# Performance work log

Measured on AMD Instinct MI355X. Metric: run time of the kernel, lower is better.

Reference implementation:

```python
import jax, jax.numpy as jnp
import numpy as np

N_USERS = 100000
N_ITEMS = 50000
N = N_USERS + N_ITEMS
EMB_DIM = 64
N_LAYERS = 3
NNZ = 6400000
BATCH = 4096


def setup_inputs() -> dict:
    key = jax.random.key(0)
    k = jax.random.split(key, 7)
    user_emb = 0.1 * jax.random.normal(k[0], (N_USERS, EMB_DIM), dtype=jnp.float32)
    item_emb = 0.1 * jax.random.normal(k[1], (N_ITEMS, EMB_DIM), dtype=jnp.float32)
    graph_val = jax.random.uniform(k[2], (NNZ,), dtype=jnp.float32) * 0.05
    graph_src = jax.random.randint(k[3], (NNZ,), 0, N, dtype=jnp.int64) if jax.config.jax_enable_x64 else jax.random.randint(k[3], (NNZ,), 0, N).astype(jnp.int32)
    graph_dst = jax.random.randint(k[4], (NNZ,), 0, N).astype(graph_src.dtype)
    users = jax.random.randint(k[5], (BATCH,), 0, N_USERS).astype(graph_src.dtype)
    items = jax.random.randint(k[6], (BATCH,), 0, N_ITEMS).astype(graph_src.dtype)
    return {"user_emb": user_emb, "item_emb": item_emb, "graph_val": graph_val,
            "graph_src": graph_src, "graph_dst": graph_dst, "users": users, "items": items}


def _spmm(val, src, dst, x):
    # y[src] += val * x[dst]  -- sparse (COO) matrix @ dense
    return jax.ops.segment_sum(val[:, None] * x[dst], src, num_segments=N)


def reference(user_emb, item_emb, graph_val, graph_src, graph_dst, users, items):
    all_emb = jnp.concatenate([user_emb, item_emb], axis=0)  # [N, d]
    acc = all_emb  # running sum over layers (fused mean accumulation)
    x = all_emb
    for _ in range(N_LAYERS):
        x = _spmm(graph_val, graph_src, graph_dst, x)
        acc = acc + x
    light_out = acc / (N_LAYERS + 1)
    all_users = light_out[:N_USERS]
    all_items = light_out[N_USERS:]
    scores = jnp.sum(all_users[users] * all_items[items], axis=1)  # [B]
    return scores
```

## Files before the change

kernel.cpp:

```cpp
#include <hip/hip_runtime.h>


constexpr int N_USERS = 100000;
constexpr int N_ITEMS = 50000;
constexpr int N_NODES = N_USERS + N_ITEMS;
constexpr int EMB = 64;
constexpr int NNZ = 6400000;
constexpr int BATCH = 4096;

constexpr int BSHIFT = 9;
constexpr int BWIDTH = 1 << BSHIFT;
constexpr int NB = (N_NODES + BWIDTH - 1) >> BSHIFT;
constexpr int NBPAD = 512;
constexpr int BSTRIDE = 23500;
constexpr int PBSTRIDE = 26624;

constexpr int TILE = 5120;
constexpr int P1_BLOCKS = NNZ / TILE;
constexpr int EPT1 = TILE / 256;

constexpr float QSCALE = 327680.0f;
constexpr float QINV   = 1.0f / 327680.0f;

struct h4 { _Float16 x, y, z, w; };
typedef _Float16 half8v __attribute__((ext_vector_type(8)));

__global__ void gcur_init_kernel(int* __restrict__ gcur) {
    int i = blockIdx.x * blockDim.x + threadIdx.x;
    if (i < NB) gcur[i] = i * BSTRIDE;
}

__global__ void p1_bin_kernel(const int* __restrict__ src, const int* __restrict__ dst,
                              const float* __restrict__ val, int* __restrict__ gcur,
                              uint2* __restrict__ staging) {
    __shared__ int hist[NBPAD];
    __shared__ int gbase[NBPAD];
    __shared__ int cur[NBPAD];
    __shared__ int sbuf[NBPAD];
    __shared__ int lbase[NBPAD];
    __shared__ uint2 ebuf[TILE];
    int t = threadIdx.x;
    int tile = blockIdx.x * TILE;
    int srcs[EPT1];
    #pragma unroll
    for (int k = 0; k < EPT1; ++k) srcs[k] = src[tile + t + k * 256];
    for (int i = t; i < NBPAD; i += 256) { hist[i] = 0; cur[i] = 0; }
    __syncthreads();
    #pragma unroll
    for (int k = 0; k < EPT1; ++k) atomicAdd(&hist[srcs[k] >> BSHIFT], 1);
    __syncthreads();
    for (int i = t; i < NB; i += 256) {
        int h = hist[i];
        gbase[i] = (h > 0) ? atomicAdd(&gcur[i], h) : 0;
    }
    for (int i = t; i < NBPAD; i += 256) sbuf[i] = hist[i];
    __syncthreads();
    int* pin = sbuf; int* pout = lbase;
    for (int off = 1; off < NBPAD; off <<= 1) {
        for (int i = t; i < NBPAD; i += 256) {
            int v = pin[i];
            if (i >= off) v += pin[i - off];
            pout[i] = v;
        }
        __syncthreads();
        int* tmp = pin; pin = pout; pout = tmp;
    }
    for (int i = t; i < NBPAD; i += 256) lbase[i] = pin[i] - hist[i];
    __syncthreads();
    #pragma unroll
    for (int k = 0; k < EPT1; ++k) {
        int i = tile + t + k * 256;
        int s = srcs[k];
        int b = s >> BSHIFT;
        int c = atomicAdd(&cur[b], 1);
        int d = dst[i];
        float v = val[i];
        unsigned q = (unsigned)(v * QSCALE);
        if (q > 16383u) q = 16383u;
        ebuf[lbase[b] + c] = make_uint2((q << 18) | (unsigned)d, (unsigned)s);
    }
    __syncthreads();
    #pragma unroll
    for (int k = 0; k < EPT1; ++k) {
        int j = t + k * 256;
        uint2 e = ebuf[j];
        int b = (int)(e.y >> BSHIFT);
        unsigned pos = (unsigned)(gbase[b] + (j - lbase[b]));
        if (pos < (unsigned)((b + 1) * BSTRIDE))
            staging[pos] = e;
    }
}

__global__ void p2_sort_kernel(const int* __restrict__ gcur, const uint2* __restrict__ staging,
                               unsigned* __restrict__ epack, unsigned* __restrict__ prow) {
    __shared__ int hist[BWIDTH], sA[BWIDTH], sB[BWIDTH], cur[BWIDTH];
    int b = blockIdx.x;
    int t = threadIdx.x;
    int cnt = gcur[b] - b * BSTRIDE;
    if (cnt > BSTRIDE) cnt = BSTRIDE;
    int sbase = b * BSTRIDE;
    for (int i = t; i < BWIDTH; i += 256) hist[i] = 0;
    __syncthreads();
    for (int j = t; j < cnt; j += 256) {
        uint2 e = staging[sbase + j];
        atomicAdd(&hist[e.y & (BWIDTH - 1)], 1);
    }
    __syncthreads();
    for (int i = t; i < BWIDTH; i += 256) sA[i] = (hist[i] + 7) >> 3;
    __syncthreads();
    int* pin = sA; int* pout = sB;
    for (int off = 1; off < BWIDTH; off <<= 1) {
        for (int i = t; i < BWIDTH; i += 256) {
            int v = pin[i];
            if (i >= off) v += pin[i - off];
            pout[i] = v;
        }
        __syncthreads();
        int* tmp = pin; pin = pout; pout = tmp;
    }
    for (int i = t; i < BWIDTH; i += 256) {
        int pw = (hist[i] + 7) >> 3;
        int ps = pin[i] - pw;
        unsigned poff = (unsigned)(b * PBSTRIDE + 8 * ps);
        int fit = (PBSTRIDE - 8 * ps) >> 3;
        if (fit < 0) fit = 0;
        if (pw > fit) pw = fit;
        if (pw > 15) pw = 15;
        cur[i] = (int)poff;
        int node = (b << BSHIFT) + i;
        if (node < N_NODES) prow[node] = (poff << 4) | (unsigned)pw;
    }
    __syncthreads();
    unsigned bend = (unsigned)((b + 1) * PBSTRIDE);
    for (int j = t; j < cnt; j += 256) {
        uint2 e = staging[sbase + j];
        int p = atomicAdd(&cur[e.y & (BWIDTH - 1)], 1);
        if ((unsigned)p < bend) epack[p] = e.x;
    }
}

__global__ void init_kernel(const float4* __restrict__ ue, const float4* __restrict__ ie,
                            h4* __restrict__ x) {
    int i = blockIdx.x * blockDim.x + threadIdx.x;
    const int total = N_NODES * (EMB / 4);
    if (i >= total) return;
    const int usplit = N_USERS * (EMB / 4);
    float4 v = (i < usplit) ? ue[i] : ie[i - usplit];
    x[i] = h4{(_Float16)v.x, (_Float16)v.y, (_Float16)v.z, (_Float16)v.w};
}

__global__ void gather_init_kernel(const float* __restrict__ ue, const float* __restrict__ ie,
                                   const int* __restrict__ users, const int* __restrict__ items,
                                   float* __restrict__ accb) {
    int gid = blockIdx.x * blockDim.x + threadIdx.x;
    int w = gid >> 6;
    int lane = threadIdx.x & 63;
    if (w >= BATCH * 2) return;
    int b = w >> 1;
    float v;
    if (w & 1) v = ie[(long long)items[b] * EMB + lane];
    else       v = ue[(long long)users[b] * EMB + lane];
    accb[(long long)w * EMB + lane] = v;
}

__global__ void gather_add_kernel(const _Float16* __restrict__ x, const int* __restrict__ users,
                                  const int* __restrict__ items, float* __restrict__ accb) {
    int gid = blockIdx.x * blockDim.x + threadIdx.x;
    int w = gid >> 6;
    int lane = threadIdx.x & 63;
    if (w >= BATCH * 2) return;
    int b = w >> 1;
    int node = (w & 1) ? (N_USERS + items[b]) : users[b];
    accb[(long long)w * EMB + lane] += (float)x[(unsigned)node * EMB + lane];
}

__device__ __forceinline__ void row_gather_p8(unsigned pr, int lane,
                                              const unsigned* __restrict__ epack,
                                              const _Float16* __restrict__ x,
                                              float acc[8]) {
    const int l8 = lane & 7;
    const int qb = lane & 56;
    const unsigned li8b = (unsigned)l8 * 16u;
    float a0 = 0, a1 = 0, a2 = 0, a3 = 0, a4 = 0, a5 = 0, a6 = 0, a7 = 0;
    float b0 = 0, b1 = 0, b2 = 0, b3 = 0, b4 = 0, b5 = 0, b6 = 0, b7 = 0;
    const unsigned* ep = epack + (pr >> 4);
    const char* xb = (const char*)x;
    int nwin = (int)(pr & 15u);
    if (nwin > 0) {
        unsigned e = ep[l8];
        for (int w = 0; w < nwin; ++w) {
            unsigned en = ep[8 + l8];
            ep += 8;
            unsigned voff = (e & 0x3FFFFu) << 7;
            float v = ((float)(e >> 18) + 0.5f) * QINV;
            #pragma unroll
            for (int t = 0; t < 8; t += 2) {
                unsigned offA = (unsigned)__shfl((int)voff, qb + t, 64);
                unsigned offB = (unsigned)__shfl((int)voff, qb + t + 1, 64);
                float vA = __shfl(v, qb + t, 64);
                float vB = __shfl(v, qb + t + 1, 64);
                const half8v hA = *(const half8v*)(xb + (offA | li8b));
                const half8v hB = *(const half8v*)(xb + (offB | li8b));
                a0 += vA * (float)hA[0];  a1 += vA * (float)hA[1];
                a2 += vA * (float)hA[2];  a3 += vA * (float)hA[3];
                a4 += vA * (float)hA[4];  a5 += vA * (float)hA[5];
                a6 += vA * (float)hA[6];  a7 += vA * (float)hA[7];
                b0 += vB * (float)hB[0];  b1 += vB * (float)hB[1];
                b2 += vB * (float)hB[2];  b3 += vB * (float)hB[3];
                b4 += vB * (float)hB[4];  b5 += vB * (float)hB[5];
                b6 += vB * (float)hB[6];  b7 += vB * (float)hB[7];
            }
            e = en;
        }
    }
    acc[0] = a0 + b0; acc[1] = a1 + b1; acc[2] = a2 + b2; acc[3] = a3 + b3;
    acc[4] = a4 + b4; acc[5] = a5 + b5; acc[6] = a6 + b6; acc[7] = a7 + b7;
}

__global__ void spmm_full_kernel(const unsigned* __restrict__ prow,
                                 const unsigned* __restrict__ epack,
                                 const _Float16* __restrict__ x, _Float16* __restrict__ y) {
    int gid = blockIdx.x * blockDim.x + threadIdx.x;
    int row = gid >> 3;
    if (row >= N_NODES) return;
    int lane = threadIdx.x & 63;
    float acc[8];
    row_gather_p8(prow[row], lane, epack, x, acc);
    half8v h;
    #pragma unroll
    for (int i = 0; i < 8; ++i) h[i] = (_Float16)acc[i];
    *(half8v*)(y + ((unsigned)row << 6) + (unsigned)(lane & 7) * 8) = h;
}

__global__ void spmm_sel_kernel(const unsigned* __restrict__ prow,
                                const unsigned* __restrict__ epack,
                                const _Float16* __restrict__ x, const int* __restrict__ users,
                                const int* __restrict__ items, float* __restrict__ accb) {
    int gid = blockIdx.x * blockDim.x + threadIdx.x;
    int g = gid >> 3;
    if (g >= BATCH * 2) return;
    int lane = threadIdx.x & 63;
    int b = g >> 1;
    int node = (g & 1) ? (N_USERS + items[b]) : users[b];
    float acc[8];
    row_gather_p8(prow[node], lane, epack, x, acc);
    float4* p = (float4*)(accb + ((long long)g << 6) + (lane & 7) * 8);
    float4 c0 = p[0], c1 = p[1];
    c0.x += acc[0]; c0.y += acc[1]; c0.z += acc[2]; c0.w += acc[3];
    c1.x += acc[4]; c1.y += acc[5]; c1.z += acc[6]; c1.w += acc[7];
    p[0] = c0; p[1] = c1;
}

__global__ void score_kernel(const float* __restrict__ accb, float* __restrict__ out) {
    int gid = blockIdx.x * blockDim.x + threadIdx.x;
    int b = gid >> 6;
    int lane = threadIdx.x & 63;
    if (b >= BATCH) return;
    float a = accb[(long long)(2 * b) * EMB + lane];
    float c = accb[(long long)(2 * b + 1) * EMB + lane];
    float p = a * c;
    #pragma unroll
    for (int off = 32; off > 0; off >>= 1) p += __shfl_down(p, off, 64);
    if (lane == 0) out[b] = p * (1.0f / 16.0f);
}

extern "C" void kernel_launch(void* const* d_in, const int* in_sizes, int n_in,
                              void* d_out, int out_size, void* d_ws, size_t ws_size,
                              hipStream_t stream) {
    const float* user_emb  = (const float*)d_in[0];
    const float* item_emb  = (const float*)d_in[1];
    const float* graph_val = (const float*)d_in[2];
    const int*   graph_src = (const int*)d_in[3];
    const int*   graph_dst = (const int*)d_in[4];
    const int*   users     = (const int*)d_in[5];
    const int*   items     = (const int*)d_in[6];
    float* out = (float*)d_out;

    char* base = (char*)d_ws;
    const size_t STAGE_BYTES = (size_t)BSTRIDE * NB * 8;
    const size_t XBYTES = (size_t)N_NODES * EMB * 2;
    const size_t PB_SLOTS = (size_t)PBSTRIDE * NB;
    uint2*    staging = (uint2*)base;
    _Float16* A       = (_Float16*)base;
    _Float16* B       = (_Float16*)(base + XBYTES);
    float*    accb    = (float*)(base + 2 * XBYTES);
    unsigned* epack   = (unsigned*)(base + STAGE_BYTES);
    unsigned* prow    = epack + PB_SLOTS;
    int*      gcur    = (int*)(prow + N_NODES);

    const int totalv4 = N_NODES * (EMB / 4);
    const int vblocks = (totalv4 + 255) / 256;
    const int wblocks = (BATCH * 2 * 64) / 256;
    const int sblocks = (N_NODES * 8 + 255) / 256;
    const int selblocks = (BATCH * 2 * 8) / 256;

    hipMemsetAsync(epack, 0, PB_SLOTS * sizeof(unsigned), stream);
    gcur_init_kernel<<<(NB + 255) / 256, 256, 0, stream>>>(gcur);
    p1_bin_kernel<<<P1_BLOCKS, 256, 0, stream>>>(graph_src, graph_dst, graph_val,
                                                 gcur, staging);
    p2_sort_kernel<<<NB, 256, 0, stream>>>(gcur, staging, epack, prow);

    init_kernel<<<vblocks, 256, 0, stream>>>((const float4*)user_emb,
                                             (const float4*)item_emb, (h4*)A);
    gather_init_kernel<<<wblocks, 256, 0, stream>>>(user_emb, item_emb, users, items, accb);

    spmm_full_kernel<<<sblocks, 256, 0, stream>>>(prow, epack, A, B);
    gather_add_kernel<<<wblocks, 256, 0, stream>>>(B, users, items, accb);

    spmm_full_kernel<<<sblocks, 256, 0, stream>>>(prow, epack, B, A);
    gather_add_kernel<<<wblocks, 256, 0, stream>>>(A, users, items, accb);

    spmm_sel_kernel<<<selblocks, 256, 0, stream>>>(prow, epack, A, users, items, accb);

    score_kernel<<<(BATCH * 64) / 256, 256, 0, stream>>>(accb, out);
}
```

Measured before the change: 521.3 us.

## Split SpMM into two feature-half passes and fold epack padding zeroing into sort

Each SpMM layer now runs as two passes, each gathering one 32-column half of the fp16 embedding rows. The aim is to halve the per-pass gather working set so it fits better in cache, at the cost of reading the edge lists twice. The sort kernel now uses 512 threads, one per bucket, and zeroes only the padding slots of each row instead of memsetting the whole epack buffer. The selected-row SpMM also gathers the two halves one after the other.

```diff
diff --git a/kernel.cpp b/kernel.cpp
--- a/kernel.cpp
+++ b/kernel.cpp
@@ -23,7 +23,7 @@
 constexpr float QINV   = 1.0f / 327680.0f;
 
 struct h4 { _Float16 x, y, z, w; };
-typedef _Float16 half8v __attribute__((ext_vector_type(8)));
+typedef _Float16 half4v __attribute__((ext_vector_type(4)));
 
 __global__ void gcur_init_kernel(int* __restrict__ gcur) {
     int i = blockIdx.x * blockDim.x + threadIdx.x;
@@ -99,40 +99,40 @@
     int cnt = gcur[b] - b * BSTRIDE;
     if (cnt > BSTRIDE) cnt = BSTRIDE;
     int sbase = b * BSTRIDE;
-    for (int i = t; i < BWIDTH; i += 256) hist[i] = 0;
-    __syncthreads();
-    for (int j = t; j < cnt; j += 256) {
+    hist[t] = 0;
+    __syncthreads();
+    for (int j = t; j < cnt; j += 512) {
         uint2 e = staging[sbase + j];
         atomicAdd(&hist[e.y & (BWIDTH - 1)], 1);
     }
     __syncthreads();
-    for (int i = t; i < BWIDTH; i += 256) sA[i] = (hist[i] + 7) >> 3;
+    sA[t] = (hist[t] + 7) >> 3;
     __syncthreads();
     int* pin = sA; int* pout = sB;
     for (int off = 1; off < BWIDTH; off <<= 1) {
-        for (int i = t; i < BWIDTH; i += 256) {
-            int v = pin[i];
-            if (i >= off) v += pin[i - off];
-            pout[i] = v;
-        }
+        int v = pin[t];
+        if (t >= off) v += pin[t - off];
+        pout[t] = v;
         __syncthreads();
         int* tmp = pin; pin = pout; pout = tmp;
     }
-    for (int i = t; i < BWIDTH; i += 256) {
-        int pw = (hist[i] + 7) >> 3;
-        int ps = pin[i] - pw;
+    {
+        int c = hist[t];
+        int pw = (c + 7) >> 3;
+        int ps = pin[t] - pw;
         unsigned poff = (unsigned)(b * PBSTRIDE + 8 * ps);
         int fit = (PBSTRIDE - 8 * ps) >> 3;
         if (fit < 0) fit = 0;
         if (pw > fit) pw = fit;
         if (pw > 15) pw = 15;
-        cur[i] = (int)poff;
-        int node = (b << BSHIFT) + i;
+        cur[t] = (int)poff;
+        int node = (b << BSHIFT) + t;
         if (node < N_NODES) prow[node] = (poff << 4) | (unsigned)pw;
+        for (int s = c; s < 8 * pw; ++s) epack[poff + s] = 0;
     }
     __syncthreads();
     unsigned bend = (unsigned)((b + 1) * PBSTRIDE);
-    for (int j = t; j < cnt; j += 256) {
+    for (int j = t; j < cnt; j += 512) {
         uint2 e = staging[sbase + j];
         int p = atomicAdd(&cur[e.y & (BWIDTH - 1)], 1);
         if ((unsigned)p < bend) epack[p] = e.x;
@@ -174,15 +174,15 @@
     accb[(long long)w * EMB + lane] += (float)x[(unsigned)node * EMB + lane];
 }
 
-__device__ __forceinline__ void row_gather_p8(unsigned pr, int lane,
-                                              const unsigned* __restrict__ epack,
-                                              const _Float16* __restrict__ x,
-                                              float acc[8]) {
+__device__ __forceinline__ void row_gather_h(unsigned pr, int lane, unsigned hb,
+                                             const unsigned* __restrict__ epack,
+                                             const _Float16* __restrict__ x,
+                                             float acc[4]) {
     const int l8 = lane & 7;
     const int qb = lane & 56;
-    const unsigned li8b = (unsigned)l8 * 16u;
-    float a0 = 0, a1 = 0, a2 = 0, a3 = 0, a4 = 0, a5 = 0, a6 = 0, a7 = 0;
-    float b0 = 0, b1 = 0, b2 = 0, b3 = 0, b4 = 0, b5 = 0, b6 = 0, b7 = 0;
+    const unsigned lib = hb | ((unsigned)l8 * 8u);
+    float a0 = 0, a1 = 0, a2 = 0, a3 = 0;
+    float b0 = 0, b1 = 0, b2 = 0, b3 = 0;
     const unsigned* ep = epack + (pr >> 4);
     const char* xb = (const char*)x;
     int nwin = (int)(pr & 15u);
@@ -199,37 +199,31 @@
                 unsigned offB = (unsigned)__shfl((int)voff, qb + t + 1, 64);
                 float vA = __shfl(v, qb + t, 64);
                 float vB = __shfl(v, qb + t + 1, 64);
-                const half8v hA = *(const half8v*)(xb + (offA | li8b));
-                const half8v hB = *(const half8v*)(xb + (offB | li8b));
+                const half4v hA = *(const half4v*)(xb + (offA | lib));
+                const half4v hB = *(const half4v*)(xb + (offB | lib));
                 a0 += vA * (float)hA[0];  a1 += vA * (float)hA[1];
                 a2 += vA * (float)hA[2];  a3 += vA * (float)hA[3];
-                a4 += vA * (float)hA[4];  a5 += vA * (float)hA[5];
-                a6 += vA * (float)hA[6];  a7 += vA * (float)hA[7];
                 b0 += vB * (float)hB[0];  b1 += vB * (float)hB[1];
                 b2 += vB * (float)hB[2];  b3 += vB * (float)hB[3];
-                b4 += vB * (float)hB[4];  b5 += vB * (float)hB[5];
-                b6 += vB * (float)hB[6];  b7 += vB * (float)hB[7];
             }
             e = en;
         }
     }
     acc[0] = a0 + b0; acc[1] = a1 + b1; acc[2] = a2 + b2; acc[3] = a3 + b3;
-    acc[4] = a4 + b4; acc[5] = a5 + b5; acc[6] = a6 + b6; acc[7] = a7 + b7;
-}
-
-__global__ void spmm_full_kernel(const unsigned* __restrict__ prow,
+}
+
+__global__ void spmm_half_kernel(const unsigned* __restrict__ prow,
                                  const unsigned* __restrict__ epack,
-                                 const _Float16* __restrict__ x, _Float16* __restrict__ y) {
+                                 const _Float16* __restrict__ x, _Float16* __restrict__ y,
+                                 unsigned hb) {
     int gid = blockIdx.x * blockDim.x + threadIdx.x;
     int row = gid >> 3;
     if (row >= N_NODES) return;
     int lane = threadIdx.x & 63;
-    float acc[8];
-    row_gather_p8(prow[row], lane, epack, x, acc);
-    half8v h;
-    #pragma unroll
-    for (int i = 0; i < 8; ++i) h[i] = (_Float16)acc[i];
-    *(half8v*)(y + ((unsigned)row << 6) + (unsigned)(lane & 7) * 8) = h;
+    float acc[4];
+    row_gather_h(prow[row], lane, hb, epack, x, acc);
+    half4v h = {(_Float16)acc[0], (_Float16)acc[1], (_Float16)acc[2], (_Float16)acc[3]};
+    *(half4v*)((char*)y + (((unsigned)row << 7) | hb | ((unsigned)(lane & 7) * 8u))) = h;
 }
 
 __global__ void spmm_sel_kernel(const unsigned* __restrict__ prow,
@@ -240,15 +234,21 @@
     int g = gid >> 3;
     if (g >= BATCH * 2) return;
     int lane = threadIdx.x & 63;
+    int l8 = lane & 7;
     int b = g >> 1;
     int node = (g & 1) ? (N_USERS + items[b]) : users[b];
-    float acc[8];
-    row_gather_p8(prow[node], lane, epack, x, acc);
-    float4* p = (float4*)(accb + ((long long)g << 6) + (lane & 7) * 8);
-    float4 c0 = p[0], c1 = p[1];
+    unsigned pr = prow[node];
+    float acc[4];
+    row_gather_h(pr, lane, 0u, epack, x, acc);
+    float4* p0 = (float4*)(accb + ((long long)g << 6) + l8 * 4);
+    float4 c0 = *p0;
     c0.x += acc[0]; c0.y += acc[1]; c0.z += acc[2]; c0.w += acc[3];
-    c1.x += acc[4]; c1.y += acc[5]; c1.z += acc[6]; c1.w += acc[7];
-    p[0] = c0; p[1] = c1;
+    *p0 = c0;
+    row_gather_h(pr, lane, 64u, epack, x, acc);
+    float4* p1 = (float4*)(accb + ((long long)g << 6) + 32 + l8 * 4);
+    float4 c1 = *p1;
+    c1.x += acc[0]; c1.y += acc[1]; c1.z += acc[2]; c1.w += acc[3];
+    *p1 = c1;
 }
 
 __global__ void score_kernel(const float* __restrict__ accb, float* __restrict__ out) {
@@ -294,20 +294,21 @@
     const int sblocks = (N_NODES * 8 + 255) / 256;
     const int selblocks = (BATCH * 2 * 8) / 256;
 
-    hipMemsetAsync(epack, 0, PB_SLOTS * sizeof(unsigned), stream);
     gcur_init_kernel<<<(NB + 255) / 256, 256, 0, stream>>>(gcur);
     p1_bin_kernel<<<P1_BLOCKS, 256, 0, stream>>>(graph_src, graph_dst, graph_val,
                                                  gcur, staging);
-    p2_sort_kernel<<<NB, 256, 0, stream>>>(gcur, staging, epack, prow);
+    p2_sort_kernel<<<NB, 512, 0, stream>>>(gcur, staging, epack, prow);
 
     init_kernel<<<vblocks, 256, 0, stream>>>((const float4*)user_emb,
                                              (const float4*)item_emb, (h4*)A);
     gather_init_kernel<<<wblocks, 256, 0, stream>>>(user_emb, item_emb, users, items, accb);
 
-    spmm_full_kernel<<<sblocks, 256, 0, stream>>>(prow, epack, A, B);
+    spmm_half_kernel<<<sblocks, 256, 0, stream>>>(prow, epack, A, B, 0u);
+    spmm_half_kernel<<<sblocks, 256, 0, stream>>>(prow, epack, A, B, 64u);
     gather_add_kernel<<<wblocks, 256, 0, stream>>>(B, users, items, accb);
 
-    spmm_full_kernel<<<sblocks, 256, 0, stream>>>(prow, epack, B, A);
+    spmm_half_kernel<<<sblocks, 256, 0, stream>>>(prow, epack, B, A, 0u);
+    spmm_half_kernel<<<sblocks, 256, 0, stream>>>(prow, epack, B, A, 64u);
     gather_add_kernel<<<wblocks, 256, 0, stream>>>(A, users, items, accb);
 
     spmm_sel_kernel<<<selblocks, 256, 0, stream>>>(prow, epack, A, users, items, accb);
```

New measurement: 710.5 us. +36.3%, slower.

## Presort binned edges by destination before row sort; drop epack memset

Applied to the files above, without the earlier changes.

Adds a counting-sort pass that orders each source bin's staged edges by destination block. The per-row sort then scatters them into epack in roughly dst order, which should improve gather locality in the SpMM passes. The full epack memset is replaced by zeroing only each row's padding slots, and p2 now runs 512 threads with one bin entry per thread. This costs an extra read and write of the staging buffer and a workspace relayout, and BSTRIDE shrinks, which makes truncation of heavy bins more likely.

```diff
diff --git a/kernel.cpp b/kernel.cpp
--- a/kernel.cpp
+++ b/kernel.cpp
@@ -12,7 +12,7 @@
 constexpr int BWIDTH = 1 << BSHIFT;
 constexpr int NB = (N_NODES + BWIDTH - 1) >> BSHIFT;
 constexpr int NBPAD = 512;
-constexpr int BSTRIDE = 23500;
+constexpr int BSTRIDE = 22500;
 constexpr int PBSTRIDE = 26624;
 
 constexpr int TILE = 5120;
@@ -91,49 +91,90 @@
     }
 }
 
-__global__ void p2_sort_kernel(const int* __restrict__ gcur, const uint2* __restrict__ staging,
+__global__ void p1p5_dsort_kernel(const int* __restrict__ gcur,
+                                  const uint2* __restrict__ staging,
+                                  uint2* __restrict__ out2) {
+    __shared__ int hist[2048], sA[2048], sB[2048], cur[2048];
+    int b = blockIdx.x;
+    int t = threadIdx.x;
+    int cnt = gcur[b] - b * BSTRIDE;
+    if (cnt > BSTRIDE) cnt = BSTRIDE;
+    if (cnt < 0) cnt = 0;
+    int sbase = b * BSTRIDE;
+    for (int i = t; i < 2048; i += 512) hist[i] = 0;
+    __syncthreads();
+    for (int j = t; j < cnt; j += 512) {
+        uint2 e = staging[sbase + j];
+        int key = (int)((e.x & 0x3FFFFu) >> 7);
+        atomicAdd(&hist[key], 1);
+    }
+    __syncthreads();
+    for (int i = t; i < 2048; i += 512) sA[i] = hist[i];
+    __syncthreads();
+    int* pin = sA; int* pout = sB;
+    for (int off = 1; off < 2048; off <<= 1) {
+        for (int i = t; i < 2048; i += 512) {
+            int v = pin[i];
+            if (i >= off) v += pin[i - off];
+            pout[i] = v;
+        }
+        __syncthreads();
+        int* tmp = pin; pin = pout; pout = tmp;
+    }
+    for (int i = t; i < 2048; i += 512) cur[i] = sbase + pin[i] - hist[i];
+    __syncthreads();
+    for (int j = t; j < cnt; j += 512) {
+        uint2 e = staging[sbase + j];
+        int key = (int)((e.x & 0x3FFFFu) >> 7);
+        int p = atomicAdd(&cur[key], 1);
+        out2[p] = e;
+    }
+}
+
+__global__ void p2_sort_kernel(const int* __restrict__ gcur, const uint2* __restrict__ out2,
                                unsigned* __restrict__ epack, unsigned* __restrict__ prow) {
     __shared__ int hist[BWIDTH], sA[BWIDTH], sB[BWIDTH], cur[BWIDTH];
     int b = blockIdx.x;
     int t = threadIdx.x;
     int cnt = gcur[b] - b * BSTRIDE;
     if (cnt > BSTRIDE) cnt = BSTRIDE;
+    if (cnt < 0) cnt = 0;
     int sbase = b * BSTRIDE;
-    for (int i = t; i < BWIDTH; i += 256) hist[i] = 0;
-    __syncthreads();
-    for (int j = t; j < cnt; j += 256) {
-        uint2 e = staging[sbase + j];
+    hist[t] = 0;
+    __syncthreads();
+    for (int j = t; j < cnt; j += 512) {
+        uint2 e = out2[sbase + j];
         atomicAdd(&hist[e.y & (BWIDTH - 1)], 1);
     }
     __syncthreads();
-    for (int i = t; i < BWIDTH; i += 256) sA[i] = (hist[i] + 7) >> 3;
+    sA[t] = (hist[t] + 7) >> 3;
     __syncthreads();
     int* pin = sA; int* pout = sB;
     for (int off = 1; off < BWIDTH; off <<= 1) {
-        for (int i = t; i < BWIDTH; i += 256) {
-            int v = pin[i];
-            if (i >= off) v += pin[i - off];
-            pout[i] = v;
-        }
+        int v = pin[t];
+        if (t >= off) v += pin[t - off];
+        pout[t] = v;
         __syncthreads();
         int* tmp = pin; pin = pout; pout = tmp;
     }
-    for (int i = t; i < BWIDTH; i += 256) {
-        int pw = (hist[i] + 7) >> 3;
-        int ps = pin[i] - pw;
+    {
+        int c = hist[t];
+        int pw = (c + 7) >> 3;
+        int ps = pin[t] - pw;
         unsigned poff = (unsigned)(b * PBSTRIDE + 8 * ps);
         int fit = (PBSTRIDE - 8 * ps) >> 3;
         if (fit < 0) fit = 0;
         if (pw > fit) pw = fit;
         if (pw > 15) pw = 15;
-        cur[i] = (int)poff;
-        int node = (b << BSHIFT) + i;
+        cur[t] = (int)poff;
+        int node = (b << BSHIFT) + t;
         if (node < N_NODES) prow[node] = (poff << 4) | (unsigned)pw;
+        for (int s = c; s < 8 * pw; ++s) epack[poff + s] = 0;
     }
     __syncthreads();
     unsigned bend = (unsigned)((b + 1) * PBSTRIDE);
-    for (int j = t; j < cnt; j += 256) {
-        uint2 e = staging[sbase + j];
+    for (int j = t; j < cnt; j += 512) {
+        uint2 e = out2[sbase + j];
         int p = atomicAdd(&cur[e.y & (BWIDTH - 1)], 1);
         if ((unsigned)p < bend) epack[p] = e.x;
     }
@@ -281,12 +322,13 @@
     const size_t XBYTES = (size_t)N_NODES * EMB * 2;
     const size_t PB_SLOTS = (size_t)PBSTRIDE * NB;
     uint2*    staging = (uint2*)base;
-    _Float16* A       = (_Float16*)base;
-    _Float16* B       = (_Float16*)(base + XBYTES);
-    float*    accb    = (float*)(base + 2 * XBYTES);
-    unsigned* epack   = (unsigned*)(base + STAGE_BYTES);
+    unsigned* epack   = (unsigned*)base;
     unsigned* prow    = epack + PB_SLOTS;
-    int*      gcur    = (int*)(prow + N_NODES);
+    uint2*    out2    = (uint2*)(base + STAGE_BYTES);
+    _Float16* A       = (_Float16*)(base + STAGE_BYTES);
+    _Float16* B       = (_Float16*)(base + STAGE_BYTES + XBYTES);
+    float*    accb    = (float*)(base + STAGE_BYTES + 2 * XBYTES);
+    int*      gcur    = (int*)(base + 2 * STAGE_BYTES);
 
     const int totalv4 = N_NODES * (EMB / 4);
     const int vblocks = (totalv4 + 255) / 256;
@@ -294,11 +336,11 @@
     const int sblocks = (N_NODES * 8 + 255) / 256;
     const int selblocks = (BATCH * 2 * 8) / 256;
 
-    hipMemsetAsync(epack, 0, PB_SLOTS * sizeof(unsigned), stream);
     gcur_init_kernel<<<(NB + 255) / 256, 256, 0, stream>>>(gcur);
     p1_bin_kernel<<<P1_BLOCKS, 256, 0, stream>>>(graph_src, graph_dst, graph_val,
                                                  gcur, staging);
-    p2_sort_kernel<<<NB, 256, 0, stream>>>(gcur, staging, epack, prow);
+    p1p5_dsort_kernel<<<NB, 512, 0, stream>>>(gcur, staging, out2);
+    p2_sort_kernel<<<NB, 512, 0, stream>>>(gcur, out2, epack, prow);
 
     init_kernel<<<vblocks, 256, 0, stream>>>((const float4*)user_emb,
                                              (const float4*)item_emb, (h4*)A);
```

After: 760.6 us. 45.9% more time.
